# Performance work log

Hardware: AMD Instinct MI355X
Metric: run time of the kernel (lower is better)

## Reference

```python
import jax, jax.numpy as jnp
from jax import lax
import numpy as np

# Config mirroring init_kwargs
B, N, PD = 4, 16384, 3
PROJ = 64                 # projection_channel
M1, K1, C1 = 2048, 32, 128  # level-1 SA: fps points, neighbors, out channel
M2, K2, C2 = 512, 32, 256   # level-2 SA
DH, DO = 512, 256           # dense hidden / out (dense_channels)


def fps(pts, M):
    """Farthest point sampling. pts: [N,3] -> indices [M] (starts at point 0)."""
    n = pts.shape[0]
    def step(carry, _):
        dmin, last = carry
        d = jnp.sum((pts - pts[last]) ** 2, axis=-1)   # dist to newest center
        dmin = jnp.minimum(dmin, d)
        nxt = jnp.argmax(dmin).astype(jnp.int32)
        return (dmin, nxt), last
    init = (jnp.full((n,), 1e10, pts.dtype), jnp.int32(0))
    _, idxs = lax.scan(step, init, None, length=M)
    return idxs


def sa_level(pts, feats, M, K, Wa, ba, Wb, bb):
    """PointNet++ set abstraction: FPS + kNN (xyz space) + grouped MLP + max."""
    idx = jax.vmap(lambda p: fps(p, M))(pts)                       # [B,M]
    centers = jnp.take_along_axis(pts, idx[:, :, None], axis=1)    # [B,M,3]
    d = jnp.sum((centers[:, :, None, :] - pts[:, None, :, :]) ** 2, -1)  # [B,M,N]
    _, nidx = lax.top_k(-d, K)                                      # [B,M,K]
    gather = jax.vmap(lambda a, i: a[i])
    rel = gather(pts, nidx) - centers[:, :, None, :]                # [B,M,K,3]
    nf = gather(feats, nidx)                                        # [B,M,K,C]
    g = jnp.concatenate([rel, nf], axis=-1)                         # use_xyz=True
    h = jax.nn.relu(g @ Wa + ba)
    h = jax.nn.relu(h @ Wb + bb)
    return centers, jnp.max(h, axis=2)                              # [B,M,Cout]


def setup_inputs() -> dict:
    key = jax.random.key(0)
    ks = jax.random.split(key, 12)
    w = lambda k, shape, s: jax.random.normal(k, shape, jnp.float32) * s
    z = lambda c: jnp.zeros((c,), jnp.float32)
    return {
        "xyz": jax.random.normal(ks[0], (B, N, PD), jnp.float32),
        "Wp": w(ks[1], (PD, PROJ), 0.3), "bp": z(PROJ),
        "W1a": w(ks[2], (PROJ + 3, C1), 0.1), "b1a": z(C1),
        "W1b": w(ks[3], (C1, C1), 0.08), "b1b": z(C1),
        "W2a": w(ks[4], (C1 + 3, C2), 0.08), "b2a": z(C2),
        "W2b": w(ks[5], (C2, C2), 0.06), "b2b": z(C2),
        "Wd1": w(ks[6], (2 * C2, DH), 0.05), "bd1": z(DH),
        "Wd2": w(ks[7], (DH, DO), 0.05), "bd2": z(DO),
    }


def reference(xyz, Wp, bp, W1a, b1a, W1b, b1b, W2a, b2a, W2b, b2b,
              Wd1, bd1, Wd2, bd2):
    feats = xyz @ Wp + bp            # point_proj: [B,N,PROJ]
    pts = xyz[..., :3]
    pts, feats = sa_level(pts, feats, M1, K1, W1a, b1a, W1b, b1b)
    pts, feats = sa_level(pts, feats, M2, K2, W2a, b2a, W2b, b2b)
    # global max + avg pool (adaptive_max/avg_pool1d to 1), concat -> [B,2*C2]
    g = jnp.concatenate([jnp.max(feats, axis=1), jnp.mean(feats, axis=1)], -1)
    h = jax.nn.relu(g @ Wd1 + bd1)   # DenseBlock w/ activation
    return h @ Wd2 + bd2             # last block: no activation (last_activation=False)
```

## Files before the change

### kernel.cpp

```cpp
#include <hip/hip_runtime.h>

#define B_    4
#define N1_   16384
#define M1_   2048
#define M2_   512
#define KNN_  32
#define PROJ_ 64
#define C1_   128
#define C2_   256
#define PROJ_BLKS_ ((B_ * N1_ * PROJ_) / 512)
#define KNN_BLKS_  ((M1_ / 64) * (B_ * 64))

__device__ __forceinline__ float sqdist_exact(float px, float py, float pz,
                                              float cx, float cy, float cz) {
    float dx = __fsub_rn(px, cx);
    float dy = __fsub_rn(py, cy);
    float dz = __fsub_rn(pz, cz);
    return __fadd_rn(__fadd_rn(__fmul_rn(dx, dx), __fmul_rn(dy, dy)), __fmul_rn(dz, dz));
}

__global__ void __launch_bounds__(1024)
sortx_kernel(const float* __restrict__ xyz, float* __restrict__ sx,
             float* __restrict__ sy, float* __restrict__ sz,
             unsigned* __restrict__ scid) {
    const int b = blockIdx.x, t = threadIdx.x;
    const int lane = t & 63, w = t >> 6;
    const float* P = xyz + (size_t)b * N1_ * 3;
    __shared__ int hist[1024];
    __shared__ int wsum[16];
    hist[t] = 0;
    __syncthreads();
    for (int j = t; j < N1_; j += 1024) {
        unsigned kb = __float_as_uint(P[j * 3]);
        kb ^= (kb >> 31) ? 0xFFFFFFFFu : 0x80000000u;
        atomicAdd(&hist[kb >> 22], 1);
    }
    __syncthreads();
    int v = hist[t];
    int cum = v;
    for (int off = 1; off < 64; off <<= 1) {
        int o = __shfl_up(cum, off);
        if (lane >= off) cum += o;
    }
    if (lane == 63) wsum[w] = cum;
    __syncthreads();
    int wpre = 0;
    for (int i = 0; i < w; ++i) wpre += wsum[i];
    const int excl = cum - v + wpre;
    __syncthreads();
    hist[t] = excl;
    __syncthreads();
    for (int j = t; j < N1_; j += 1024) {
        float x = P[j * 3], y = P[j * 3 + 1], z = P[j * 3 + 2];
        unsigned kb = __float_as_uint(x);
        kb ^= (kb >> 31) ? 0xFFFFFFFFu : 0x80000000u;
        int pos = atomicAdd(&hist[kb >> 22], 1);
        size_t o = (size_t)b * N1_ + pos;
        sx[o] = x; sy[o] = y; sz[o] = z; scid[o] = ~(unsigned)j;
    }
}

typedef float v2f __attribute__((ext_vector_type(2)));

template<int CTRL, int RM>
__device__ __forceinline__ unsigned long long dpp_umax64(unsigned long long pk) {
    unsigned lo = (unsigned)__builtin_amdgcn_update_dpp(
        0, (int)(unsigned)pk, CTRL, RM, 0xf, true);
    unsigned hi = (unsigned)__builtin_amdgcn_update_dpp(
        0, (int)(unsigned)(pk >> 32), CTRL, RM, 0xf, true);
    unsigned long long o = ((unsigned long long)hi << 32) | (unsigned long long)lo;
    return (o > pk) ? o : pk;
}

__device__ __forceinline__ unsigned long long wave_max_key(unsigned long long pk) {
    pk = dpp_umax64<0x111, 0xf>(pk);
    pk = dpp_umax64<0x112, 0xf>(pk);
    pk = dpp_umax64<0x114, 0xf>(pk);
    pk = dpp_umax64<0x118, 0xf>(pk);
    pk = dpp_umax64<0x142, 0xa>(pk);
    pk = dpp_umax64<0x143, 0xc>(pk);
    return pk;
}

__device__ __forceinline__ unsigned reduce8_widx(const unsigned long long* wk,
                                                 int lane) {
    unsigned long long k8 = wk[lane & 7];
    k8 = dpp_umax64<0x111, 0xf>(k8);
    k8 = dpp_umax64<0x112, 0xf>(k8);
    k8 = dpp_umax64<0x114, 0xf>(k8);
    unsigned lo = (unsigned)__builtin_amdgcn_readlane((int)(unsigned)k8, 7);
    return ~lo;
}

__device__ __forceinline__ unsigned reduce2_widx(const unsigned long long* wk,
                                                 int lane) {
    unsigned long long k2 = wk[lane & 1];
    k2 = dpp_umax64<0x111, 0xf>(k2);
    unsigned lo = (unsigned)__builtin_amdgcn_readlane((int)(unsigned)k2, 1);
    return ~lo;
}

template<int N>
__device__ void knn_body512(const float* __restrict__ P,
                            float cx, float cy, float cz,
                            int* __restrict__ out, char* arena) {
    constexpr int K = KNN_;
    constexpr int CAP = 224;
    const int t = threadIdx.x;
    const int lane = t & 63;
    const int w = t >> 6;

    int*      hist = (int*)arena;
    unsigned* eqk  = (unsigned*)(arena + 8192);
    int*      eqi  = (int*)(arena + 8192 + 896);
    int*      wsum = (int*)(arena + 8192 + 1792);
    int*      ctrl = (int*)(arena + 8192 + 1824);

    unsigned prefix = 0; int pbits = 0;
    unsigned Tlo = 0; unsigned long long Thi = 0x100000000ull;
    int L = 0, target = K, Cbin = N;

    for (int round = 0; round < 3; ++round) {
        const int bits  = (round < 2) ? 11 : 10;
        const int nbins = 1 << bits;
        const int shift = 32 - pbits - bits;
        for (int i = t; i < nbins; i += 512) hist[i] = 0;
        __syncthreads();
        for (int j = t; j < N; j += 512) {
            float d = sqdist_exact(P[j * 3], P[j * 3 + 1], P[j * 3 + 2], cx, cy, cz);
            unsigned key = __float_as_uint(d);
            if (key >= Tlo && (unsigned long long)key < Thi)
                atomicAdd(&hist[(key >> shift) & (nbins - 1)], 1);
        }
        __syncthreads();
        const int per = nbins / 512;
        int s = 0;
        for (int i = 0; i < per; ++i) s += hist[t * per + i];
        int cum = s;
        for (int off = 1; off < 64; off <<= 1) {
            int o = __shfl_up(cum, off);
            if (lane >= off) cum += o;
        }
        if (lane == 63) wsum[w] = cum;
        __syncthreads();
        int wpre = 0;
        for (int i = 0; i < w; ++i) wpre += wsum[i];
        cum += wpre;
        const int cumex = cum - s;
        if ((cumex < target) && (cum >= target)) {
            int acc = cumex;
            for (int i = 0; i < per; ++i) {
                int h = hist[t * per + i];
                if (acc + h >= target) { ctrl[2] = t * per + i; ctrl[3] = acc; ctrl[4] = h; break; }
                acc += h;
            }
        }
        __syncthreads();
        const int binsel = ctrl[2];
        const int Ladd   = ctrl[3];
        const int bincnt = ctrl[4];
        L += Ladd;
        target -= Ladd;
        prefix = (prefix << bits) | (unsigned)binsel;
        pbits += bits;
        Tlo = prefix << (32 - pbits);
        Thi = ((unsigned long long)prefix + 1ull) << (32 - pbits);
        Cbin = bincnt;
        __syncthreads();
        if (Cbin <= CAP) break;
    }

    if (t == 0) { ctrl[0] = 0; ctrl[1] = 0; }
    __syncthreads();

    if (Cbin <= CAP) {
        for (int j = t; j < N; j += 512) {
            float d = sqdist_exact(P[j * 3], P[j * 3 + 1], P[j * 3 + 2], cx, cy, cz);
            unsigned key = __float_as_uint(d);
            if (key < Tlo) {
                int p = atomicAdd(&ctrl[0], 1);
                out[p] = j;
            } else if ((unsigned long long)key < Thi) {
                int p = atomicAdd(&ctrl[1], 1);
                eqk[p] = key; eqi[p] = j;
            }
        }
        __syncthreads();
        const int E = ctrl[1];
        for (int e = t; e < E; e += 512) {
            unsigned ke = eqk[e]; int ie = eqi[e];
            int rank = 0;
            for (int f = 0; f < E; ++f) {
                unsigned kf = eqk[f]; int jf = eqi[f];
                rank += (kf < ke || (kf == ke && jf < ie)) ? 1 : 0;
            }
            if (rank < target) out[L + rank] = ie;
        }
    } else {
        if (t < 64) {
            int cnt = 0;
            for (int jb = 0; jb < N; jb += 64) {
                int j = jb + lane;
                float d = sqdist_exact(P[j * 3], P[j * 3 + 1], P[j * 3 + 2], cx, cy, cz);
                unsigned key = __float_as_uint(d);
                if (key < Tlo) {
                    int p = atomicAdd(&ctrl[0], 1);
                    out[p] = j;
                }
                bool eq = (key == Tlo);
                unsigned long long mb = __ballot(eq);
                int below = __popcll(mb & ((1ull << lane) - 1ull));
                if (eq && (cnt + below) < target) out[L + cnt + below] = j;
                cnt += (int)__popcll(mb);
            }
        }
    }
}

__global__ __attribute__((amdgpu_flat_work_group_size(512, 512)))
__attribute__((amdgpu_waves_per_eu(2, 2)))
void mega1_kernel(const float* __restrict__ xyz,
                  const float* __restrict__ sx, const float* __restrict__ sy,
                  const float* __restrict__ sz, const unsigned* __restrict__ scid,
                  const float* __restrict__ Wp, const float* __restrict__ bp,
                  float* __restrict__ feats0, float* __restrict__ centers1,
                  int* __restrict__ nidx1, unsigned* __restrict__ prog) {
#pragma clang fp contract(off)
    __shared__ alignas(16) char arena[24832];
    asm volatile("" ::: "v255");
    const int bid = blockIdx.x;
    const int t = threadIdx.x;

    if (bid >= B_ + PROJ_BLKS_) {
        const int k = bid - (B_ + PROJ_BLKS_);
        const int c = k >> 8;
        const int b = (k >> 6) & 3;
        const int m = c * 64 + (k & 63);
        if (t == 0) {
            while (__hip_atomic_load(&prog[b * 16], __ATOMIC_RELAXED,
                                     __HIP_MEMORY_SCOPE_AGENT) <= (unsigned)c)
                __builtin_amdgcn_s_sleep(16);
        }
        __syncthreads();
        const unsigned* cw = (const unsigned*)(centers1 + ((size_t)b * M1_ + m) * 3);
        float cx = __uint_as_float(__hip_atomic_load(cw + 0, __ATOMIC_RELAXED, __HIP_MEMORY_SCOPE_AGENT));
        float cy = __uint_as_float(__hip_atomic_load(cw + 1, __ATOMIC_RELAXED, __HIP_MEMORY_SCOPE_AGENT));
        float cz = __uint_as_float(__hip_atomic_load(cw + 2, __ATOMIC_RELAXED, __HIP_MEMORY_SCOPE_AGENT));
        knn_body512<N1_>(xyz + (size_t)b * N1_ * 3, cx, cy, cz,
                         nidx1 + ((size_t)b * M1_ + m) * KNN_, arena);
        return;
    }
    if (bid >= B_) {
        int tid = (bid - B_) * 512 + t;
        int cc = tid & (PROJ_ - 1);
        int pn = tid >> 6;
        const float* p = xyz + (size_t)pn * 3;
        float acc = p[0] * Wp[0 * PROJ_ + cc];
        acc = __fmaf_rn(p[1], Wp[1 * PROJ_ + cc], acc);
        acc = __fmaf_rn(p[2], Wp[2 * PROJ_ + cc], acc);
        feats0[tid] = acc + bp[cc];
        return;
    }
    constexpr int NT = 512;
    constexpr int NW = NT / 64;
    constexpr int PPT = N1_ / NT;
    const int b = bid;
    const int w = t >> 6;
    const int lane = t & 63;
    const float* P  = xyz + (size_t)b * N1_ * 3;
    const float* SX = sx + (size_t)b * N1_;
    const float* SY = sy + (size_t)b * N1_;
    const float* SZ = sz + (size_t)b * N1_;
    const unsigned* SC = scid + (size_t)b * N1_;
    float* C1 = centers1 + (size_t)b * M1_ * 3;
    const int base = t * PPT;

    unsigned long long (*wkey)[NW] = (unsigned long long(*)[NW])arena;
    float* cb1 = (float*)(arena + 128);

    float px[PPT], py[PPT], pz[PPT], dmin[PPT];
#pragma unroll
    for (int k = 0; k < PPT; ++k) {
        px[k] = SX[base + k];
        py[k] = SY[base + k];
        pz[k] = SZ[base + k];
        dmin[k] = 1e10f;
    }
#pragma unroll
    for (int k = 0; k < PPT; ++k)
        asm volatile("" : "+v"(px[k]), "+v"(py[k]), "+v"(pz[k]), "+v"(dmin[k]));

    float xlo = px[0], xhi = px[0];
#pragma unroll
    for (int k = 1; k < PPT; ++k) {
        xlo = fminf(xlo, px[k]);
        xhi = fmaxf(xhi, px[k]);
    }
    for (int off = 1; off < 64; off <<= 1) {
        xlo = fminf(xlo, __shfl_xor(xlo, off));
        xhi = fmaxf(xhi, __shfl_xor(xhi, off));
    }

    unsigned long long mykey = ((unsigned long long)__float_as_uint(1e10f) << 32);
    float cx = P[0], cy = P[1], cz = P[2];

    for (int m = 0; m < M1_; ++m) {
        if (t == 0) {
            cb1[m * 3 + 0] = cx; cb1[m * 3 + 1] = cy; cb1[m * 3 + 2] = cz;
        }
        if ((m & 63) == 63) {
            __syncthreads();
            const int c = m >> 6;
            if (t < 48)
                ((float4*)C1)[c * 48 + t] = ((const float4*)cb1)[c * 48 + t];
            __syncthreads();
            if (t == 0)
                __hip_atomic_store(&prog[b * 16], (unsigned)(c + 1),
                                   __ATOMIC_RELEASE, __HIP_MEMORY_SCOPE_AGENT);
        }
        if (m == M1_ - 1) break;
        const int par = m & 1;
        const float UBval = __uint_as_float((unsigned)(mykey >> 32));
        const float dxs = fmaxf(fmaxf(xlo - cx, cx - xhi), 0.0f);
        if (!(0.999f * (dxs * dxs) >= UBval)) {
            unsigned long long pk = 0;
#pragma unroll
            for (int k = 0; k < PPT; ++k) {
                float d  = sqdist_exact(px[k], py[k], pz[k], cx, cy, cz);
                float nd = fminf(dmin[k], d);
                dmin[k] = nd;
                unsigned long long kk =
                    ((unsigned long long)__float_as_uint(nd) << 32) | SC[base + k];
                pk = (kk > pk) ? kk : pk;
            }
            pk = wave_max_key(pk);
            unsigned klo = (unsigned)__builtin_amdgcn_readlane((int)(unsigned)pk, 63);
            unsigned khi = (unsigned)__builtin_amdgcn_readlane((int)(unsigned)(pk >> 32), 63);
            mykey = ((unsigned long long)khi << 32) | klo;
        }
        if (lane == 63) wkey[par][w] = mykey;
        __syncthreads();
        const unsigned widx = reduce8_widx(wkey[par], lane);
        const float* cp = P + (size_t)widx * 3;
        cx = cp[0]; cy = cp[1]; cz = cp[2];
    }
}

__device__ __forceinline__ void fps2_body(const float* __restrict__ centers1,
                                          float* __restrict__ centers2,
                                          char* arena) {
#pragma clang fp contract(off)
    constexpr int NT = 128;
    constexpr int NW = 2;
    constexpr int NP = (M1_ / NT) / 2;
    const int b = blockIdx.x;
    const int t = threadIdx.x;
    const int w = t >> 6;
    const int lane = t & 63;
    const float* P = centers1 + (size_t)b * M1_ * 3;
    float* C = centers2 + (size_t)b * M2_ * 3;

    unsigned long long (*wkey)[NW] = (unsigned long long(*)[NW])arena;
    float* cb2 = (float*)(arena + 64);

    v2f px2[NP], py2[NP], pz2[NP];
    float dmin[2 * NP];
#pragma unroll
    for (int p = 0; p < NP; ++p) {
        const int j0 = (2 * p) * NT + t;
        const int j1 = j0 + NT;
        px2[p] = (v2f){P[j0 * 3 + 0], P[j1 * 3 + 0]};
        py2[p] = (v2f){P[j0 * 3 + 1], P[j1 * 3 + 1]};
        pz2[p] = (v2f){P[j0 * 3 + 2], P[j1 * 3 + 2]};
        dmin[2 * p] = 1e10f; dmin[2 * p + 1] = 1e10f;
    }
#pragma unroll
    for (int p = 0; p < NP; ++p)
        asm volatile("" : "+v"(px2[p]), "+v"(py2[p]), "+v"(pz2[p]));

    float cx = P[0], cy = P[1], cz = P[2];

    for (int m = 0; m < M2_; ++m) {
        if (t == 0) {
            cb2[m * 3 + 0] = cx; cb2[m * 3 + 1] = cy; cb2[m * 3 + 2] = cz;
        }
        if (m == M2_ - 1) break;
        const int par = m & 1;
        const v2f c2x = {cx, cx}, c2y = {cy, cy}, c2z = {cz, cz};
        float bv = -1.0f; int bk = 0;
#pragma unroll
        for (int p = 0; p < NP; ++p) {
            v2f dx = px2[p] - c2x;
            v2f dy = py2[p] - c2y;
            v2f dz = pz2[p] - c2z;
            v2f d2 = (dx * dx + dy * dy) + dz * dz;
            float nd0 = fminf(dmin[2 * p],     d2.x);
            float nd1 = fminf(dmin[2 * p + 1], d2.y);
            dmin[2 * p]     = nd0;
            dmin[2 * p + 1] = nd1;
            bool g0 = nd0 > bv; bv = g0 ? nd0 : bv; bk = g0 ? 2 * p     : bk;
            bool g1 = nd1 > bv; bv = g1 ? nd1 : bv; bk = g1 ? 2 * p + 1 : bk;
        }
        unsigned gi = (unsigned)(bk * NT + t);
        unsigned long long pk =
            ((unsigned long long)__float_as_uint(bv) << 32) | (unsigned)(~gi);
        pk = wave_max_key(pk);
        if (lane == 63) wkey[par][w] = pk;
        __syncthreads();
        const unsigned widx = reduce2_widx(wkey[par], lane);
        const float* cp = P + (size_t)widx * 3;
        cx = cp[0]; cy = cp[1]; cz = cp[2];
    }
    __syncthreads();
#pragma unroll 1
    for (int i = t; i < (M2_ * 3) / 4; i += NT)
        ((float4*)C)[i] = ((const float4*)cb2)[i];
}

template<int NPTS, int FD, int CO, int M>
__device__ __forceinline__ void mlp_body(int bm, char* arena,
                 const float* __restrict__ pts, const float* __restrict__ feats,
                 const float* __restrict__ centers, const int* __restrict__ nidx,
                 const float* __restrict__ Wa, const float* __restrict__ ba,
                 const float* __restrict__ Wb, const float* __restrict__ bb,
                 float* __restrict__ outf) {
    constexpr int KN = KNN_;
    constexpr int GS = FD + 4;
    const int b = bm / M;
    const int t = threadIdx.x;
    float (*g)[GS]  = (float(*)[GS])arena;
    float (*h1)[CO] = (float(*)[CO])(arena + sizeof(float) * KN * GS);
    const int* nb = nidx + (size_t)bm * KN;
    const float* cen = centers + (size_t)bm * 3;
    const float cx = cen[0], cy = cen[1], cz = cen[2];
    {
        constexpr int PARTS = CO / KN;
        constexpr int CHUNK = FD / PARTS;
        const int kk = t / PARTS;
        const int q  = t % PARTS;
        const int j  = nb[kk];
        const float* f = feats + ((size_t)b * NPTS + j) * FD + q * CHUNK;
        float* gr = &g[kk][q * CHUNK];
#pragma unroll
        for (int u = 0; u < CHUNK / 4; ++u)
            *(float4*)(gr + 4 * u) = *(const float4*)(f + 4 * u);
        if (q == 0) {
            const float* p = pts + ((size_t)b * NPTS + j) * 3;
            g[kk][FD + 0] = __fsub_rn(p[0], cx);
            g[kk][FD + 1] = __fsub_rn(p[1], cy);
            g[kk][FD + 2] = __fsub_rn(p[2], cz);
            g[kk][FD + 3] = 0.f;
        }
    }
    __syncthreads();
    const int o = t;
    float acc[KN];
#pragma unroll
    for (int k = 0; k < KN; ++k) acc[k] = ba[o];
    for (int s4 = 0; s4 < FD / 4; ++s4) {
        const float w0 = Wa[(4 * s4 + 3) * CO + o];
        const float w1 = Wa[(4 * s4 + 4) * CO + o];
        const float w2 = Wa[(4 * s4 + 5) * CO + o];
        const float w3 = Wa[(4 * s4 + 6) * CO + o];
#pragma unroll
        for (int k = 0; k < KN; ++k) {
            float4 gv = *(const float4*)&g[k][4 * s4];
            acc[k] = __fmaf_rn(gv.x, w0, acc[k]);
            acc[k] = __fmaf_rn(gv.y, w1, acc[k]);
            acc[k] = __fmaf_rn(gv.z, w2, acc[k]);
            acc[k] = __fmaf_rn(gv.w, w3, acc[k]);
        }
    }
    {
        const float w0 = Wa[0 * CO + o];
        const float w1 = Wa[1 * CO + o];
        const float w2 = Wa[2 * CO + o];
#pragma unroll
        for (int k = 0; k < KN; ++k) {
            float4 gv = *(const float4*)&g[k][FD];
            acc[k] = __fmaf_rn(gv.x, w0, acc[k]);
            acc[k] = __fmaf_rn(gv.y, w1, acc[k]);
            acc[k] = __fmaf_rn(gv.z, w2, acc[k]);
        }
    }
#pragma unroll
    for (int k = 0; k < KN; ++k) h1[k][o] = fmaxf(acc[k], 0.f);
    __syncthreads();
#pragma unroll
    for (int k = 0; k < KN; ++k) acc[k] = bb[o];
    for (int s4 = 0; s4 < CO / 4; ++s4) {
        const float w0 = Wb[(4 * s4 + 0) * CO + o];
        const float w1 = Wb[(4 * s4 + 1) * CO + o];
        const float w2 = Wb[(4 * s4 + 2) * CO + o];
        const float w3 = Wb[(4 * s4 + 3) * CO + o];
#pragma unroll
        for (int k = 0; k < KN; ++k) {
            float4 hv = *(const float4*)&h1[k][4 * s4];
            acc[k] = __fmaf_rn(hv.x, w0, acc[k]);
            acc[k] = __fmaf_rn(hv.y, w1, acc[k]);
            acc[k] = __fmaf_rn(hv.z, w2, acc[k]);
            acc[k] = __fmaf_rn(hv.w, w3, acc[k]);
        }
    }
    float mx = 0.f;
#pragma unroll
    for (int k = 0; k < KN; ++k) mx = fmaxf(mx, fmaxf(acc[k], 0.f));
    outf[(size_t)bm * CO + o] = mx;
}

__global__ void __launch_bounds__(C1_)
sa1_kernel(const float* __restrict__ xyz, const float* __restrict__ feats0,
           const float* __restrict__ centers1, const int* __restrict__ nidx1,
           const float* __restrict__ W1a, const float* __restrict__ b1a,
           const float* __restrict__ W1b, const float* __restrict__ b1b,
           float* __restrict__ feats1, float* __restrict__ centers2) {
    constexpr size_t MLP_BYTES =
        sizeof(float) * (KNN_ * (PROJ_ + 4) + KNN_ * C1_);
    __shared__ alignas(16) char arena[MLP_BYTES];
    if (blockIdx.x < B_) {
        fps2_body(centers1, centers2, arena);
        return;
    }
    mlp_body<N1_, PROJ_, C1_, M1_>(blockIdx.x - B_, arena, xyz, feats0,
                                   centers1, nidx1, W1a, b1a, W1b, b1b, feats1);
}

template<int NPTS, int FD, int CO, int M>
__global__ void __launch_bounds__(CO)
group_mlp_kernel(const float* __restrict__ pts, const float* __restrict__ feats,
                 const float* __restrict__ centers, const int* __restrict__ nidx,
                 const float* __restrict__ Wa, const float* __restrict__ ba,
                 const float* __restrict__ Wb, const float* __restrict__ bb,
                 float* __restrict__ outf) {
    constexpr size_t BYTES = sizeof(float) * (KNN_ * (FD + 4) + KNN_ * CO);
    __shared__ alignas(16) char arena[BYTES];
    mlp_body<NPTS, FD, CO, M>(blockIdx.x, arena, pts, feats, centers, nidx,
                              Wa, ba, Wb, bb, outf);
}

template<int N, int M>
__global__ void __launch_bounds__(64)
knn_kernel(const float* __restrict__ pts, const float* __restrict__ centers,
           int* __restrict__ nidx) {
    constexpr int K = KNN_;
    constexpr int CAP = 224;
    const int bm = blockIdx.x;
    const int b = bm / M;
    const int lane = threadIdx.x;
    const float* P = pts + (size_t)b * N * 3;
    const float* c = centers + (size_t)bm * 3;
    const float cx = c[0], cy = c[1], cz = c[2];
    int* out = nidx + (size_t)bm * K;

    __shared__ int hist[2048];
    __shared__ unsigned int eqk[CAP];
    __shared__ int eqi[CAP];
    __shared__ int cnt_less, cnt_eq;

    unsigned int prefix = 0; int pbits = 0;
    unsigned int Tlo = 0; unsigned long long Thi = 0x100000000ull;
    int L = 0, target = K, Cbin = N;

    for (int round = 0; round < 3; ++round) {
        const int bits  = (round < 2) ? 11 : 10;
        const int nbins = 1 << bits;
        const int shift = 32 - pbits - bits;
        for (int i = lane; i < nbins; i += 64) hist[i] = 0;
        __syncthreads();
        for (int j = lane; j < N; j += 64) {
            float d = sqdist_exact(P[j * 3], P[j * 3 + 1], P[j * 3 + 2], cx, cy, cz);
            unsigned int key = __float_as_uint(d);
            if (key >= Tlo && (unsigned long long)key < Thi)
                atomicAdd(&hist[(key >> shift) & (nbins - 1)], 1);
        }
        __syncthreads();
        const int per = nbins / 64;
        int s = 0;
        for (int i = 0; i < per; ++i) s += hist[lane * per + i];
        int cum = s;
        for (int off = 1; off < 64; off <<= 1) {
            int o = __shfl_up(cum, off);
            if (lane >= off) cum += o;
        }
        int cumex = cum - s;
        bool has = (cumex < target) && (cum >= target);
        unsigned long long ball = __ballot(has);
        int src = __ffsll(ball) - 1;
        int binsel = 0, Ladd = 0, bincnt = 0;
        if (lane == src) {
            int acc = cumex;
            for (int i = 0; i < per; ++i) {
                int h = hist[lane * per + i];
                if (acc + h >= target) { binsel = lane * per + i; Ladd = acc; bincnt = h; break; }
                acc += h;
            }
        }
        binsel = __shfl(binsel, src);
        Ladd   = __shfl(Ladd, src);
        bincnt = __shfl(bincnt, src);
        L += Ladd;
        target -= Ladd;
        prefix = (prefix << bits) | (unsigned int)binsel;
        pbits += bits;
        Tlo = prefix << (32 - pbits);
        Thi = ((unsigned long long)prefix + 1ull) << (32 - pbits);
        Cbin = bincnt;
        __syncthreads();
        if (Cbin <= CAP) break;
    }

    if (lane == 0) { cnt_less = 0; cnt_eq = 0; }
    __syncthreads();

    if (Cbin <= CAP) {
        for (int j = lane; j < N; j += 64) {
            float d = sqdist_exact(P[j * 3], P[j * 3 + 1], P[j * 3 + 2], cx, cy, cz);
            unsigned int key = __float_as_uint(d);
            if (key < Tlo) {
                int p = atomicAdd(&cnt_less, 1);
                out[p] = j;
            } else if ((unsigned long long)key < Thi) {
                int p = atomicAdd(&cnt_eq, 1);
                eqk[p] = key; eqi[p] = j;
            }
        }
        __syncthreads();
        const int E = cnt_eq;
        for (int e = lane; e < E; e += 64) {
            unsigned int ke = eqk[e]; int ie = eqi[e];
            int rank = 0;
            for (int f = 0; f < E; ++f) {
                unsigned int kf = eqk[f]; int jf = eqi[f];
                rank += (kf < ke || (kf == ke && jf < ie)) ? 1 : 0;
            }
            if (rank < target) out[L + rank] = ie;
        }
    } else {
        int cnt = 0;
        for (int jb = 0; jb < N; jb += 64) {
            int j = jb + lane;
            float d = sqdist_exact(P[j * 3], P[j * 3 + 1], P[j * 3 + 2], cx, cy, cz);
            unsigned int key = __float_as_uint(d);
            if (key < Tlo) {
                int p = atomicAdd(&cnt_less, 1);
                out[p] = j;
            }
            bool eq = (key == Tlo);
            unsigned long long mb = __ballot(eq);
            int below = __popcll(mb & ((1ull << lane) - 1ull));
            if (eq && (cnt + below) < target) out[L + cnt + below] = j;
            cnt += (int)__popcll(mb);
        }
    }
}

__global__ void __launch_bounds__(256)
head_kernel(const float* __restrict__ feats2,
            const float* __restrict__ Wd1, const float* __restrict__ bd1,
            const float* __restrict__ Wd2, const float* __restrict__ bd2,
            float* __restrict__ outp) {
    const int b = blockIdx.x, t = threadIdx.x;
    __shared__ float gsh[2 * C2_];
    __shared__ float hsh[512];
    const float* F = feats2 + (size_t)b * M2_ * C2_;
    float mx = -1e30f, sm = 0.f;
    for (int r = 0; r < M2_; ++r) {
        float v = F[r * C2_ + t];
        mx = fmaxf(mx, v);
        sm += v;
    }
    gsh[t] = mx;
    gsh[C2_ + t] = sm * (1.0f / (float)M2_);
    __syncthreads();
#pragma unroll
    for (int oo = 0; oo < 2; ++oo) {
        const int o = t + oo * 256;
        float acc = bd1[o];
        for (int i = 0; i < 512; ++i)
            acc = __fmaf_rn(gsh[i], Wd1[i * 512 + o], acc);
        hsh[o] = fmaxf(acc, 0.f);
    }
    __syncthreads();
    float acc = bd2[t];
    for (int i = 0; i < 512; ++i)
        acc = __fmaf_rn(hsh[i], Wd2[i * 256 + t], acc);
    outp[b * 256 + t] = acc;
}

extern "C" void kernel_launch(void* const* d_in, const int* in_sizes, int n_in,
                              void* d_out, int out_size, void* d_ws, size_t ws_size,
                              hipStream_t stream) {
    const float* xyz = (const float*)d_in[0];
    const float* Wp  = (const float*)d_in[1];
    const float* bp  = (const float*)d_in[2];
    const float* W1a = (const float*)d_in[3];
    const float* b1a = (const float*)d_in[4];
    const float* W1b = (const float*)d_in[5];
    const float* b1b = (const float*)d_in[6];
    const float* W2a = (const float*)d_in[7];
    const float* b2a = (const float*)d_in[8];
    const float* W2b = (const float*)d_in[9];
    const float* b2b = (const float*)d_in[10];
    const float* Wd1 = (const float*)d_in[11];
    const float* bd1 = (const float*)d_in[12];
    const float* Wd2 = (const float*)d_in[13];
    const float* bd2 = (const float*)d_in[14];
    float* out = (float*)d_out;

    char* ws = (char*)d_ws;
    size_t off = 0;
    auto alloc = [&](size_t bytes) { void* p = ws + off; off += (bytes + 255) & ~(size_t)255; return p; };
    float* feats0   = (float*)alloc((size_t)B_ * N1_ * PROJ_ * 4);
    float* centers1 = (float*)alloc((size_t)B_ * M1_ * 3 * 4);
    int*   nidx1    = (int*)  alloc((size_t)B_ * M1_ * KNN_ * 4);
    float* feats1   = (float*)alloc((size_t)B_ * M1_ * C1_ * 4);
    float* centers2 = (float*)alloc((size_t)B_ * M2_ * 3 * 4);
    int*   nidx2    = (int*)  alloc((size_t)B_ * M2_ * KNN_ * 4);
    float* feats2   = (float*)alloc((size_t)B_ * M2_ * C2_ * 4);
    unsigned* prog  = (unsigned*)alloc(B_ * 16 * 4);
    float* sx       = (float*)alloc((size_t)B_ * N1_ * 4);
    float* sy       = (float*)alloc((size_t)B_ * N1_ * 4);
    float* sz       = (float*)alloc((size_t)B_ * N1_ * 4);
    unsigned* scid  = (unsigned*)alloc((size_t)B_ * N1_ * 4);
    (void)in_sizes; (void)n_in; (void)out_size; (void)ws_size;

    hipMemsetAsync(prog, 0, B_ * 16 * 4, stream);

    sortx_kernel<<<dim3(B_), dim3(1024), 0, stream>>>(xyz, sx, sy, sz, scid);
    mega1_kernel<<<dim3(B_ + PROJ_BLKS_ + KNN_BLKS_), dim3(512), 0, stream>>>(
        xyz, sx, sy, sz, scid, Wp, bp, feats0, centers1, nidx1, prog);
    sa1_kernel<<<dim3(B_ + B_ * M1_), dim3(C1_), 0, stream>>>(
        xyz, feats0, centers1, nidx1, W1a, b1a, W1b, b1b, feats1, centers2);
    knn_kernel<M1_, M2_><<<dim3(B_ * M2_), dim3(64), 0, stream>>>(centers1, centers2, nidx2);
    group_mlp_kernel<M1_, C1_, C2_, M2_><<<dim3(B_ * M2_), dim3(C2_), 0, stream>>>(
        centers1, feats1, centers2, nidx2, W2a, b2a, W2b, b2b, feats2);
    head_kernel<<<dim3(B_), dim3(256), 0, stream>>>(feats2, Wd1, bd1, Wd2, bd2, out);
}
```

Before: 3.768 ms.

## Sort points by Morton code and prune FPS waves with 3D bounding boxes

```diff
diff --git a/kernel.cpp b/kernel.cpp
--- a/kernel.cpp
+++ b/kernel.cpp
@@ -19,8 +19,17 @@
     return __fadd_rn(__fadd_rn(__fmul_rn(dx, dx), __fmul_rn(dy, dy)), __fmul_rn(dz, dz));
 }
 
+__device__ __forceinline__ unsigned spread3(unsigned v) {
+    v &= 0x3FFu;
+    v = (v | (v << 16)) & 0x030000FFu;
+    v = (v | (v << 8))  & 0x0300F00Fu;
+    v = (v | (v << 4))  & 0x030C30C3u;
+    v = (v | (v << 2))  & 0x09249249u;
+    return v;
+}
+
 __global__ void __launch_bounds__(1024)
-sortx_kernel(const float* __restrict__ xyz, float* __restrict__ sx,
+sortm_kernel(const float* __restrict__ xyz, float* __restrict__ sx,
              float* __restrict__ sy, float* __restrict__ sz,
              unsigned* __restrict__ scid) {
     const int b = blockIdx.x, t = threadIdx.x;
@@ -28,12 +37,50 @@
     const float* P = xyz + (size_t)b * N1_ * 3;
     __shared__ int hist[1024];
     __shared__ int wsum[16];
+    __shared__ float wred[16][6];
+    __shared__ float bb[6];
+
+    float mnx = 1e30f, mxx = -1e30f, mny = 1e30f, mxy = -1e30f,
+          mnz = 1e30f, mxz = -1e30f;
+    for (int j = t; j < N1_; j += 1024) {
+        float x = P[j * 3], y = P[j * 3 + 1], z = P[j * 3 + 2];
+        mnx = fminf(mnx, x); mxx = fmaxf(mxx, x);
+        mny = fminf(mny, y); mxy = fmaxf(mxy, y);
+        mnz = fminf(mnz, z); mxz = fmaxf(mxz, z);
+    }
+    for (int off = 1; off < 64; off <<= 1) {
+        mnx = fminf(mnx, __shfl_xor(mnx, off)); mxx = fmaxf(mxx, __shfl_xor(mxx, off));
+        mny = fminf(mny, __shfl_xor(mny, off)); mxy = fmaxf(mxy, __shfl_xor(mxy, off));
+        mnz = fminf(mnz, __shfl_xor(mnz, off)); mxz = fmaxf(mxz, __shfl_xor(mxz, off));
+    }
+    if (lane == 0) {
+        wred[w][0] = mnx; wred[w][1] = mxx; wred[w][2] = mny;
+        wred[w][3] = mxy; wred[w][4] = mnz; wred[w][5] = mxz;
+    }
+    __syncthreads();
+    if (t == 0) {
+        float a0 = wred[0][0], a1 = wred[0][1], a2 = wred[0][2],
+              a3 = wred[0][3], a4 = wred[0][4], a5 = wred[0][5];
+        for (int i = 1; i < 16; ++i) {
+            a0 = fminf(a0, wred[i][0]); a1 = fmaxf(a1, wred[i][1]);
+            a2 = fminf(a2, wred[i][2]); a3 = fmaxf(a3, wred[i][3]);
+            a4 = fminf(a4, wred[i][4]); a5 = fmaxf(a5, wred[i][5]);
+        }
+        bb[0] = a0; bb[1] = a1; bb[2] = a2; bb[3] = a3; bb[4] = a4; bb[5] = a5;
+    }
     hist[t] = 0;
     __syncthreads();
+    const float ox = bb[0], oy = bb[2], oz = bb[4];
+    const float scx = 1023.0f / fmaxf(bb[1] - bb[0], 1e-20f);
+    const float scy = 1023.0f / fmaxf(bb[3] - bb[2], 1e-20f);
+    const float scz = 1023.0f / fmaxf(bb[5] - bb[4], 1e-20f);
+
     for (int j = t; j < N1_; j += 1024) {
-        unsigned kb = __float_as_uint(P[j * 3]);
-        kb ^= (kb >> 31) ? 0xFFFFFFFFu : 0x80000000u;
-        atomicAdd(&hist[kb >> 22], 1);
+        unsigned qx = (unsigned)fminf((P[j * 3 + 0] - ox) * scx, 1023.f);
+        unsigned qy = (unsigned)fminf((P[j * 3 + 1] - oy) * scy, 1023.f);
+        unsigned qz = (unsigned)fminf((P[j * 3 + 2] - oz) * scz, 1023.f);
+        unsigned code = (spread3(qx) << 2) | (spread3(qy) << 1) | spread3(qz);
+        atomicAdd(&hist[code >> 20], 1);
     }
     __syncthreads();
     int v = hist[t];
@@ -52,9 +99,11 @@
     __syncthreads();
     for (int j = t; j < N1_; j += 1024) {
         float x = P[j * 3], y = P[j * 3 + 1], z = P[j * 3 + 2];
-        unsigned kb = __float_as_uint(x);
-        kb ^= (kb >> 31) ? 0xFFFFFFFFu : 0x80000000u;
-        int pos = atomicAdd(&hist[kb >> 22], 1);
+        unsigned qx = (unsigned)fminf((x - ox) * scx, 1023.f);
+        unsigned qy = (unsigned)fminf((y - oy) * scy, 1023.f);
+        unsigned qz = (unsigned)fminf((z - oz) * scz, 1023.f);
+        unsigned code = (spread3(qx) << 2) | (spread3(qy) << 1) | spread3(qz);
+        int pos = atomicAdd(&hist[code >> 20], 1);
         size_t o = (size_t)b * N1_ + pos;
         sx[o] = x; sy[o] = y; sz[o] = z; scid[o] = ~(unsigned)j;
     }
@@ -273,32 +322,39 @@
     const float* SZ = sz + (size_t)b * N1_;
     const unsigned* SC = scid + (size_t)b * N1_;
     float* C1 = centers1 + (size_t)b * M1_ * 3;
-    const int base = t * PPT;
+    const int slab = (w & 3) * 2 + (w >> 2);
+    const int base = slab * (N1_ / NW) + lane * PPT;
 
     unsigned long long (*wkey)[NW] = (unsigned long long(*)[NW])arena;
     float* cb1 = (float*)(arena + 128);
 
     float px[PPT], py[PPT], pz[PPT], dmin[PPT];
+    unsigned cid[PPT];
 #pragma unroll
     for (int k = 0; k < PPT; ++k) {
         px[k] = SX[base + k];
         py[k] = SY[base + k];
         pz[k] = SZ[base + k];
+        cid[k] = SC[base + k];
         dmin[k] = 1e10f;
     }
 #pragma unroll
     for (int k = 0; k < PPT; ++k)
-        asm volatile("" : "+v"(px[k]), "+v"(py[k]), "+v"(pz[k]), "+v"(dmin[k]));
-
-    float xlo = px[0], xhi = px[0];
+        asm volatile("" : "+v"(px[k]), "+v"(py[k]), "+v"(pz[k]),
+                          "+v"(dmin[k]), "+v"(cid[k]));
+
+    float xlo = px[0], xhi = px[0], ylo = py[0], yhi = py[0],
+          zlo = pz[0], zhi = pz[0];
 #pragma unroll
     for (int k = 1; k < PPT; ++k) {
-        xlo = fminf(xlo, px[k]);
-        xhi = fmaxf(xhi, px[k]);
+        xlo = fminf(xlo, px[k]); xhi = fmaxf(xhi, px[k]);
+        ylo = fminf(ylo, py[k]); yhi = fmaxf(yhi, py[k]);
+        zlo = fminf(zlo, pz[k]); zhi = fmaxf(zhi, pz[k]);
     }
     for (int off = 1; off < 64; off <<= 1) {
-        xlo = fminf(xlo, __shfl_xor(xlo, off));
-        xhi = fmaxf(xhi, __shfl_xor(xhi, off));
+        xlo = fminf(xlo, __shfl_xor(xlo, off)); xhi = fmaxf(xhi, __shfl_xor(xhi, off));
+        ylo = fminf(ylo, __shfl_xor(ylo, off)); yhi = fmaxf(yhi, __shfl_xor(yhi, off));
+        zlo = fminf(zlo, __shfl_xor(zlo, off)); zhi = fmaxf(zhi, __shfl_xor(zhi, off));
     }
 
     unsigned long long mykey = ((unsigned long long)__float_as_uint(1e10f) << 32);
@@ -321,8 +377,11 @@
         if (m == M1_ - 1) break;
         const int par = m & 1;
         const float UBval = __uint_as_float((unsigned)(mykey >> 32));
-        const float dxs = fmaxf(fmaxf(xlo - cx, cx - xhi), 0.0f);
-        if (!(0.999f * (dxs * dxs) >= UBval)) {
+        const float ddx = fmaxf(fmaxf(xlo - cx, cx - xhi), 0.0f);
+        const float ddy = fmaxf(fmaxf(ylo - cy, cy - yhi), 0.0f);
+        const float ddz = fmaxf(fmaxf(zlo - cz, cz - zhi), 0.0f);
+        const float bd2 = ddx * ddx + ddy * ddy + ddz * ddz;
+        if (!(0.999f * bd2 >= UBval)) {
             unsigned long long pk = 0;
 #pragma unroll
             for (int k = 0; k < PPT; ++k) {
@@ -330,7 +389,7 @@
                 float nd = fminf(dmin[k], d);
                 dmin[k] = nd;
                 unsigned long long kk =
-                    ((unsigned long long)__float_as_uint(nd) << 32) | SC[base + k];
+                    ((unsigned long long)__float_as_uint(nd) << 32) | cid[k];
                 pk = (kk > pk) ? kk : pk;
             }
             pk = wave_max_key(pk);
@@ -726,7 +785,7 @@
 
     hipMemsetAsync(prog, 0, B_ * 16 * 4, stream);
 
-    sortx_kernel<<<dim3(B_), dim3(1024), 0, stream>>>(xyz, sx, sy, sz, scid);
+    sortm_kernel<<<dim3(B_), dim3(1024), 0, stream>>>(xyz, sx, sy, sz, scid);
     mega1_kernel<<<dim3(B_ + PROJ_BLKS_ + KNN_BLKS_), dim3(512), 0, stream>>>(
         xyz, sx, sy, sz, scid, Wp, bp, feats0, centers1, nidx1, prog);
     sa1_kernel<<<dim3(B_ + B_ * M1_), dim3(C1_), 0, stream>>>(
```

Result: slower. 4.111 ms (+9.1%).

## Overlap level-2 kNN with FPS2 via progress flags and fuse MLP2 with head

Applied to the files above, without the earlier changes.

```diff
diff --git a/kernel.cpp b/kernel.cpp
--- a/kernel.cpp
+++ b/kernel.cpp
@@ -19,6 +19,18 @@
     return __fadd_rn(__fadd_rn(__fmul_rn(dx, dx), __fmul_rn(dy, dy)), __fmul_rn(dz, dz));
 }
 
+__device__ __forceinline__ float aload(const float* p) {
+    return __uint_as_float(__hip_atomic_load((const unsigned*)p,
+                           __ATOMIC_RELAXED, __HIP_MEMORY_SCOPE_AGENT));
+}
+__device__ __forceinline__ unsigned auload(const unsigned* p) {
+    return __hip_atomic_load(p, __ATOMIC_RELAXED, __HIP_MEMORY_SCOPE_AGENT);
+}
+
+#define F_PROG1(f,b) ((f) + (b) * 16)
+#define F_PROG2(f,b) ((f) + 64 + (b) * 16)
+#define F_M2DONE(f,b) ((f) + 128 + (b) * 16)
+
 __global__ void __launch_bounds__(1024)
 sortx_kernel(const float* __restrict__ xyz, float* __restrict__ sx,
              float* __restrict__ sy, float* __restrict__ sz,
@@ -100,12 +112,13 @@
     return ~lo;
 }
 
-template<int N>
-__device__ void knn_body512(const float* __restrict__ P,
-                            float cx, float cy, float cz,
-                            int* __restrict__ out, char* arena) {
+template<int N, int NT>
+__device__ void knn_bodyT(const float* __restrict__ P,
+                          float cx, float cy, float cz,
+                          int* __restrict__ out, char* arena) {
     constexpr int K = KNN_;
     constexpr int CAP = 224;
+    constexpr int NWV = NT / 64;
     const int t = threadIdx.x;
     const int lane = t & 63;
     const int w = t >> 6;
@@ -124,16 +137,16 @@
         const int bits  = (round < 2) ? 11 : 10;
         const int nbins = 1 << bits;
         const int shift = 32 - pbits - bits;
-        for (int i = t; i < nbins; i += 512) hist[i] = 0;
-        __syncthreads();
-        for (int j = t; j < N; j += 512) {
+        for (int i = t; i < nbins; i += NT) hist[i] = 0;
+        __syncthreads();
+        for (int j = t; j < N; j += NT) {
             float d = sqdist_exact(P[j * 3], P[j * 3 + 1], P[j * 3 + 2], cx, cy, cz);
             unsigned key = __float_as_uint(d);
             if (key >= Tlo && (unsigned long long)key < Thi)
                 atomicAdd(&hist[(key >> shift) & (nbins - 1)], 1);
         }
         __syncthreads();
-        const int per = nbins / 512;
+        const int per = nbins / NT;
         int s = 0;
         for (int i = 0; i < per; ++i) s += hist[t * per + i];
         int cum = s;
@@ -174,7 +187,7 @@
     __syncthreads();
 
     if (Cbin <= CAP) {
-        for (int j = t; j < N; j += 512) {
+        for (int j = t; j < N; j += NT) {
             float d = sqdist_exact(P[j * 3], P[j * 3 + 1], P[j * 3 + 2], cx, cy, cz);
             unsigned key = __float_as_uint(d);
             if (key < Tlo) {
@@ -187,7 +200,7 @@
         }
         __syncthreads();
         const int E = ctrl[1];
-        for (int e = t; e < E; e += 512) {
+        for (int e = t; e < E; e += NT) {
             unsigned ke = eqk[e]; int ie = eqi[e];
             int rank = 0;
             for (int f = 0; f < E; ++f) {
@@ -237,17 +250,14 @@
         const int b = (k >> 6) & 3;
         const int m = c * 64 + (k & 63);
         if (t == 0) {
-            while (__hip_atomic_load(&prog[b * 16], __ATOMIC_RELAXED,
-                                     __HIP_MEMORY_SCOPE_AGENT) <= (unsigned)c)
+            while (auload(F_PROG1(prog, b)) <= (unsigned)c)
                 __builtin_amdgcn_s_sleep(16);
         }
         __syncthreads();
-        const unsigned* cw = (const unsigned*)(centers1 + ((size_t)b * M1_ + m) * 3);
-        float cx = __uint_as_float(__hip_atomic_load(cw + 0, __ATOMIC_RELAXED, __HIP_MEMORY_SCOPE_AGENT));
-        float cy = __uint_as_float(__hip_atomic_load(cw + 1, __ATOMIC_RELAXED, __HIP_MEMORY_SCOPE_AGENT));
-        float cz = __uint_as_float(__hip_atomic_load(cw + 2, __ATOMIC_RELAXED, __HIP_MEMORY_SCOPE_AGENT));
-        knn_body512<N1_>(xyz + (size_t)b * N1_ * 3, cx, cy, cz,
-                         nidx1 + ((size_t)b * M1_ + m) * KNN_, arena);
+        const float* cw = centers1 + ((size_t)b * M1_ + m) * 3;
+        float cx = aload(cw + 0), cy = aload(cw + 1), cz = aload(cw + 2);
+        knn_bodyT<N1_, 512>(xyz + (size_t)b * N1_ * 3, cx, cy, cz,
+                            nidx1 + ((size_t)b * M1_ + m) * KNN_, arena);
         return;
     }
     if (bid >= B_) {
@@ -315,7 +325,7 @@
                 ((float4*)C1)[c * 48 + t] = ((const float4*)cb1)[c * 48 + t];
             __syncthreads();
             if (t == 0)
-                __hip_atomic_store(&prog[b * 16], (unsigned)(c + 1),
+                __hip_atomic_store(F_PROG1(prog, b), (unsigned)(c + 1),
                                    __ATOMIC_RELEASE, __HIP_MEMORY_SCOPE_AGENT);
         }
         if (m == M1_ - 1) break;
@@ -348,6 +358,7 @@
 
 __device__ __forceinline__ void fps2_body(const float* __restrict__ centers1,
                                           float* __restrict__ centers2,
+                                          unsigned* __restrict__ prog,
                                           char* arena) {
 #pragma clang fp contract(off)
     constexpr int NT = 128;
@@ -384,6 +395,16 @@
         if (t == 0) {
             cb2[m * 3 + 0] = cx; cb2[m * 3 + 1] = cy; cb2[m * 3 + 2] = cz;
         }
+        if ((m & 63) == 63) {
+            __syncthreads();
+            const int c = m >> 6;
+            if (t < 48)
+                ((float4*)C)[c * 48 + t] = ((const float4*)cb2)[c * 48 + t];
+            __syncthreads();
+            if (t == 0)
+                __hip_atomic_store(F_PROG2(prog, b), (unsigned)(c + 1),
+                                   __ATOMIC_RELEASE, __HIP_MEMORY_SCOPE_AGENT);
+        }
         if (m == M2_ - 1) break;
         const int par = m & 1;
         const v2f c2x = {cx, cx}, c2y = {cy, cy}, c2z = {cz, cz};
@@ -411,10 +432,6 @@
         const float* cp = P + (size_t)widx * 3;
         cx = cp[0]; cy = cp[1]; cz = cp[2];
     }
-    __syncthreads();
-#pragma unroll 1
-    for (int i = t; i < (M2_ * 3) / 4; i += NT)
-        ((float4*)C)[i] = ((const float4*)cb2)[i];
 }
 
 template<int NPTS, int FD, int CO, int M>
@@ -513,159 +530,73 @@
            const float* __restrict__ centers1, const int* __restrict__ nidx1,
            const float* __restrict__ W1a, const float* __restrict__ b1a,
            const float* __restrict__ W1b, const float* __restrict__ b1b,
-           float* __restrict__ feats1, float* __restrict__ centers2) {
+           float* __restrict__ feats1, float* __restrict__ centers2,
+           int* __restrict__ nidx2, unsigned* __restrict__ prog) {
     constexpr size_t MLP_BYTES =
         sizeof(float) * (KNN_ * (PROJ_ + 4) + KNN_ * C1_);
     __shared__ alignas(16) char arena[MLP_BYTES];
-    if (blockIdx.x < B_) {
-        fps2_body(centers1, centers2, arena);
+    const int bid = blockIdx.x;
+    const int t = threadIdx.x;
+    if (bid < B_) {
+        fps2_body(centers1, centers2, prog, arena);
         return;
     }
-    mlp_body<N1_, PROJ_, C1_, M1_>(blockIdx.x - B_, arena, xyz, feats0,
-                                   centers1, nidx1, W1a, b1a, W1b, b1b, feats1);
-}
-
-template<int NPTS, int FD, int CO, int M>
-__global__ void __launch_bounds__(CO)
-group_mlp_kernel(const float* __restrict__ pts, const float* __restrict__ feats,
-                 const float* __restrict__ centers, const int* __restrict__ nidx,
-                 const float* __restrict__ Wa, const float* __restrict__ ba,
-                 const float* __restrict__ Wb, const float* __restrict__ bb,
-                 float* __restrict__ outf) {
-    constexpr size_t BYTES = sizeof(float) * (KNN_ * (FD + 4) + KNN_ * CO);
+    if (bid < B_ + B_ * M1_) {
+        mlp_body<N1_, PROJ_, C1_, M1_>(bid - B_, arena, xyz, feats0,
+                                       centers1, nidx1, W1a, b1a, W1b, b1b, feats1);
+        return;
+    }
+    const int k = bid - (B_ + B_ * M1_);
+    const int c = k >> 8;
+    const int b = (k >> 6) & 3;
+    const int m = c * 64 + (k & 63);
+    if (t == 0) {
+        while (auload(F_PROG2(prog, b)) <= (unsigned)c)
+            __builtin_amdgcn_s_sleep(16);
+    }
+    __syncthreads();
+    const float* cw = centers2 + ((size_t)b * M2_ + m) * 3;
+    float cx = aload(cw + 0), cy = aload(cw + 1), cz = aload(cw + 2);
+    knn_bodyT<M1_, 128>(centers1 + (size_t)b * M1_ * 3, cx, cy, cz,
+                        nidx2 + ((size_t)b * M2_ + m) * KNN_, arena);
+}
+
+__global__ void __launch_bounds__(C2_)
+mlp2_head_kernel(const float* __restrict__ centers1, const float* __restrict__ feats1,
+                 const float* __restrict__ centers2, const int* __restrict__ nidx2,
+                 const float* __restrict__ W2a, const float* __restrict__ b2a,
+                 const float* __restrict__ W2b, const float* __restrict__ b2b,
+                 const float* __restrict__ Wd1, const float* __restrict__ bd1,
+                 const float* __restrict__ Wd2, const float* __restrict__ bd2,
+                 float* __restrict__ feats2, float* __restrict__ outp,
+                 unsigned* __restrict__ prog) {
+    constexpr size_t BYTES = sizeof(float) * (KNN_ * (C1_ + 4) + KNN_ * C2_);
     __shared__ alignas(16) char arena[BYTES];
-    mlp_body<NPTS, FD, CO, M>(blockIdx.x, arena, pts, feats, centers, nidx,
-                              Wa, ba, Wb, bb, outf);
-}
-
-template<int N, int M>
-__global__ void __launch_bounds__(64)
-knn_kernel(const float* __restrict__ pts, const float* __restrict__ centers,
-           int* __restrict__ nidx) {
-    constexpr int K = KNN_;
-    constexpr int CAP = 224;
-    const int bm = blockIdx.x;
-    const int b = bm / M;
-    const int lane = threadIdx.x;
-    const float* P = pts + (size_t)b * N * 3;
-    const float* c = centers + (size_t)bm * 3;
-    const float cx = c[0], cy = c[1], cz = c[2];
-    int* out = nidx + (size_t)bm * K;
-
-    __shared__ int hist[2048];
-    __shared__ unsigned int eqk[CAP];
-    __shared__ int eqi[CAP];
-    __shared__ int cnt_less, cnt_eq;
-
-    unsigned int prefix = 0; int pbits = 0;
-    unsigned int Tlo = 0; unsigned long long Thi = 0x100000000ull;
-    int L = 0, target = K, Cbin = N;
-
-    for (int round = 0; round < 3; ++round) {
-        const int bits  = (round < 2) ? 11 : 10;
-        const int nbins = 1 << bits;
-        const int shift = 32 - pbits - bits;
-        for (int i = lane; i < nbins; i += 64) hist[i] = 0;
-        __syncthreads();
-        for (int j = lane; j < N; j += 64) {
-            float d = sqdist_exact(P[j * 3], P[j * 3 + 1], P[j * 3 + 2], cx, cy, cz);
-            unsigned int key = __float_as_uint(d);
-            if (key >= Tlo && (unsigned long long)key < Thi)
-                atomicAdd(&hist[(key >> shift) & (nbins - 1)], 1);
-        }
-        __syncthreads();
-        const int per = nbins / 64;
-        int s = 0;
-        for (int i = 0; i < per; ++i) s += hist[lane * per + i];
-        int cum = s;
-        for (int off = 1; off < 64; off <<= 1) {
-            int o = __shfl_up(cum, off);
-            if (lane >= off) cum += o;
-        }
-        int cumex = cum - s;
-        bool has = (cumex < target) && (cum >= target);
-        unsigned long long ball = __ballot(has);
-        int src = __ffsll(ball) - 1;
-        int binsel = 0, Ladd = 0, bincnt = 0;
-        if (lane == src) {
-            int acc = cumex;
-            for (int i = 0; i < per; ++i) {
-                int h = hist[lane * per + i];
-                if (acc + h >= target) { binsel = lane * per + i; Ladd = acc; bincnt = h; break; }
-                acc += h;
-            }
-        }
-        binsel = __shfl(binsel, src);
-        Ladd   = __shfl(Ladd, src);
-        bincnt = __shfl(bincnt, src);
-        L += Ladd;
-        target -= Ladd;
-        prefix = (prefix << bits) | (unsigned int)binsel;
-        pbits += bits;
-        Tlo = prefix << (32 - pbits);
-        Thi = ((unsigned long long)prefix + 1ull) << (32 - pbits);
-        Cbin = bincnt;
-        __syncthreads();
-        if (Cbin <= CAP) break;
-    }
-
-    if (lane == 0) { cnt_less = 0; cnt_eq = 0; }
-    __syncthreads();
-
-    if (Cbin <= CAP) {
-        for (int j = lane; j < N; j += 64) {
-            float d = sqdist_exact(P[j * 3], P[j * 3 + 1], P[j * 3 + 2], cx, cy, cz);
-            unsigned int key = __float_as_uint(d);
-            if (key < Tlo) {
-                int p = atomicAdd(&cnt_less, 1);
-                out[p] = j;
-            } else if ((unsigned long long)key < Thi) {
-                int p = atomicAdd(&cnt_eq, 1);
-                eqk[p] = key; eqi[p] = j;
-            }
-        }
-        __syncthreads();
-        const int E = cnt_eq;
-        for (int e = lane; e < E; e += 64) {
-            unsigned int ke = eqk[e]; int ie = eqi[e];
-            int rank = 0;
-            for (int f = 0; f < E; ++f) {
-                unsigned int kf = eqk[f]; int jf = eqi[f];
-                rank += (kf < ke || (kf == ke && jf < ie)) ? 1 : 0;
-            }
-            if (rank < target) out[L + rank] = ie;
-        }
-    } else {
-        int cnt = 0;
-        for (int jb = 0; jb < N; jb += 64) {
-            int j = jb + lane;
-            float d = sqdist_exact(P[j * 3], P[j * 3 + 1], P[j * 3 + 2], cx, cy, cz);
-            unsigned int key = __float_as_uint(d);
-            if (key < Tlo) {
-                int p = atomicAdd(&cnt_less, 1);
-                out[p] = j;
-            }
-            bool eq = (key == Tlo);
-            unsigned long long mb = __ballot(eq);
-            int below = __popcll(mb & ((1ull << lane) - 1ull));
-            if (eq && (cnt + below) < target) out[L + cnt + below] = j;
-            cnt += (int)__popcll(mb);
-        }
-    }
-}
-
-__global__ void __launch_bounds__(256)
-head_kernel(const float* __restrict__ feats2,
-            const float* __restrict__ Wd1, const float* __restrict__ bd1,
-            const float* __restrict__ Wd2, const float* __restrict__ bd2,
-            float* __restrict__ outp) {
-    const int b = blockIdx.x, t = threadIdx.x;
-    __shared__ float gsh[2 * C2_];
-    __shared__ float hsh[512];
+    const int bid = blockIdx.x;
+    const int t = threadIdx.x;
+    if (bid < B_ * M2_) {
+        mlp_body<M1_, C1_, C2_, M2_>(bid, arena, centers1, feats1,
+                                     centers2, nidx2, W2a, b2a, W2b, b2b, feats2);
+        __syncthreads();
+        if (t == 0) {
+            const int b = bid / M2_;
+            __hip_atomic_fetch_add(F_M2DONE(prog, b), 1u,
+                                   __ATOMIC_RELEASE, __HIP_MEMORY_SCOPE_AGENT);
+        }
+        return;
+    }
+    const int b = bid - B_ * M2_;
+    if (t == 0) {
+        while (auload(F_M2DONE(prog, b)) < (unsigned)M2_)
+            __builtin_amdgcn_s_sleep(16);
+    }
+    __syncthreads();
+    float* gsh = (float*)arena;
+    float* hsh = (float*)(arena + 2048);
     const float* F = feats2 + (size_t)b * M2_ * C2_;
     float mx = -1e30f, sm = 0.f;
     for (int r = 0; r < M2_; ++r) {
-        float v = F[r * C2_ + t];
+        float v = aload(&F[r * C2_ + t]);
         mx = fmaxf(mx, v);
         sm += v;
     }
@@ -717,22 +648,22 @@
     float* centers2 = (float*)alloc((size_t)B_ * M2_ * 3 * 4);
     int*   nidx2    = (int*)  alloc((size_t)B_ * M2_ * KNN_ * 4);
     float* feats2   = (float*)alloc((size_t)B_ * M2_ * C2_ * 4);
-    unsigned* prog  = (unsigned*)alloc(B_ * 16 * 4);
+    unsigned* prog  = (unsigned*)alloc(1024);
     float* sx       = (float*)alloc((size_t)B_ * N1_ * 4);
     float* sy       = (float*)alloc((size_t)B_ * N1_ * 4);
     float* sz       = (float*)alloc((size_t)B_ * N1_ * 4);
     unsigned* scid  = (unsigned*)alloc((size_t)B_ * N1_ * 4);
     (void)in_sizes; (void)n_in; (void)out_size; (void)ws_size;
 
-    hipMemsetAsync(prog, 0, B_ * 16 * 4, stream);
+    hipMemsetAsync(prog, 0, 1024, stream);
 
     sortx_kernel<<<dim3(B_), dim3(1024), 0, stream>>>(xyz, sx, sy, sz, scid);
     mega1_kernel<<<dim3(B_ + PROJ_BLKS_ + KNN_BLKS_), dim3(512), 0, stream>>>(
         xyz, sx, sy, sz, scid, Wp, bp, feats0, centers1, nidx1, prog);
-    sa1_kernel<<<dim3(B_ + B_ * M1_), dim3(C1_), 0, stream>>>(
-        xyz, feats0, centers1, nidx1, W1a, b1a, W1b, b1b, feats1, centers2);
-    knn_kernel<M1_, M2_><<<dim3(B_ * M2_), dim3(64), 0, stream>>>(centers1, centers2, nidx2);
-    group_mlp_kernel<M1_, C1_, C2_, M2_><<<dim3(B_ * M2_), dim3(C2_), 0, stream>>>(
-        centers1, feats1, centers2, nidx2, W2a, b2a, W2b, b2b, feats2);
-    head_kernel<<<dim3(B_), dim3(256), 0, stream>>>(feats2, Wd1, bd1, Wd2, bd2, out);
-}
+    sa1_kernel<<<dim3(B_ + B_ * M1_ + B_ * M2_), dim3(C1_), 0, stream>>>(
+        xyz, feats0, centers1, nidx1, W1a, b1a, W1b, b1b, feats1,
+        centers2, nidx2, prog);
+    mlp2_head_kernel<<<dim3(B_ * M2_ + B_), dim3(C2_), 0, stream>>>(
+        centers1, feats1, centers2, nidx2, W2a, b2a, W2b, b2b,
+        Wd1, bd1, Wd2, bd2, feats2, out, prog);
+}
```

Result: no change. 3.797 ms (+0.8%).
